# Kernel optimization log

Measured on AMD Instinct MI355X. Metric: run time of the kernel, lower is better.

Reference implementation:

```python
import jax, jax.numpy as jnp
import numpy as np
import math

B, S, D = 2, 512, 768
N_HEADS, HEAD = 12, 64
ALPHA = 32.0


def setup_inputs() -> dict:
    key = jax.random.key(0)
    ks = jax.random.split(key, 12)
    w_scale = 1.0 / math.sqrt(D)
    return {
        "hidden_states": jax.random.normal(ks[0], (B, S, D), jnp.float32),
        "attention_mask": jnp.zeros((B, 1, 1, S), jnp.float32),
        "rel_pos": jax.random.normal(ks[1], (B, S, S, HEAD), jnp.float32),
        "rel_2d_pos": jax.random.normal(ks[2], (B, S, S, HEAD), jnp.float32),
        "rel_2d_angle": jax.random.normal(ks[3], (B, S, S, HEAD), jnp.float32),
        "Wq": jax.random.normal(ks[4], (D, D), jnp.float32) * w_scale,
        "bq": jnp.zeros((D,), jnp.float32),
        "Wk": jax.random.normal(ks[5], (D, D), jnp.float32) * w_scale,
        "bk": jnp.zeros((D,), jnp.float32),
        "Wv": jax.random.normal(ks[6], (D, D), jnp.float32) * w_scale,
        "bv": jnp.zeros((D,), jnp.float32),
    }


def _heads(x):
    # (B,S,D) -> (B,N,S,HEAD)
    b, s, _ = x.shape
    return x.reshape(b, s, N_HEADS, HEAD).transpose(0, 2, 1, 3)


def reference(hidden_states, attention_mask, rel_pos, rel_2d_pos, rel_2d_angle,
              Wq, bq, Wk, bk, Wv, bv):
    q = _heads(hidden_states @ Wq.T + bq)
    k = _heads(hidden_states @ Wk.T + bk)
    v = _heads(hidden_states @ Wv.T + bv)

    qs = q / math.sqrt(HEAD)  # scaled query, (B,N,S,HEAD)
    scores = jnp.einsum('bnsh,bnkh->bnsk', qs, k)
    scores = scores + jnp.einsum('bnsh,bskh->bnsk', qs, rel_pos)
    scores = scores + jnp.einsum('bnsh,bskh->bnsk', qs, rel_2d_pos)
    scores = scores + jnp.einsum('bnsh,bskh->bnsk', qs, rel_2d_angle)
    scores = scores + attention_mask

    # cogview (PB-Relax) softmax: subtract per-row max of scores/alpha, rescale
    scaled = scores / ALPHA
    m = jnp.max(scaled, axis=-1, keepdims=True)
    probs = jax.nn.softmax((scaled - m) * ALPHA, axis=-1)

    ctx = jnp.einsum('bnsk,bnkh->bsnh', probs, v)  # (B,S,N,HEAD)
    return ctx.reshape(ctx.shape[0], ctx.shape[1], N_HEADS * HEAD)
```

## Files before the change

kernel.cpp:

```cpp
#include <hip/hip_runtime.h>

typedef __attribute__((ext_vector_type(8))) short short8;
typedef __attribute__((ext_vector_type(4))) float f32x4;

#define B_ 2
#define S_ 512
#define D_ 768
#define NH 12
#define HD 64

__device__ inline short f2bf(float f) {
    union { float f; unsigned u; } v; v.f = f;
    unsigned r = v.u + 0x7fffu + ((v.u >> 16) & 1u);
    return (short)(r >> 16);
}

__device__ __forceinline__ f32x4 ntload4(const float* p) {
    return __builtin_nontemporal_load((const f32x4*)p);
}

__global__ __launch_bounds__(256) void qkv_gemm(
    const float* __restrict__ hidden,
    const float* __restrict__ Wq, const float* __restrict__ Wk, const float* __restrict__ Wv,
    const float* __restrict__ bq, const float* __restrict__ bk, const float* __restrict__ bv,
    short* __restrict__ qbf, short* __restrict__ kbf, float* __restrict__ vws)
{
    __shared__ short hs[64 * 72];
    __shared__ short wt[64 * 72];

    const int mt = blockIdx.x, nt = blockIdx.y, mat = blockIdx.z;
    const int m0 = mt * 64, n0 = nt * 64;
    const float* W    = (mat == 0) ? Wq : ((mat == 1) ? Wk : Wv);
    const float* bias = (mat == 0) ? bq : ((mat == 1) ? bk : bv);

    const int tid = threadIdx.x;
    const int w = tid >> 6, l = tid & 63;
    const int sr = tid >> 2, sc = (tid & 3) * 16;

    f32x4 acc[4];
    #pragma unroll
    for (int i = 0; i < 4; ++i) acc[i] = (f32x4){0.f, 0.f, 0.f, 0.f};

    const int arow = (w * 16 + (l & 15)) * 72 + (l >> 4) * 8;

    for (int kt = 0; kt < 12; ++kt) {
        const int d0 = kt * 64;
        if (kt) __syncthreads();
        {
            const float4* sa = (const float4*)(hidden + (size_t)(m0 + sr) * D_ + d0 + sc);
            float4 x0 = sa[0], x1 = sa[1], x2 = sa[2], x3 = sa[3];
            short8 p0 = {f2bf(x0.x), f2bf(x0.y), f2bf(x0.z), f2bf(x0.w),
                         f2bf(x1.x), f2bf(x1.y), f2bf(x1.z), f2bf(x1.w)};
            short8 p1 = {f2bf(x2.x), f2bf(x2.y), f2bf(x2.z), f2bf(x2.w),
                         f2bf(x3.x), f2bf(x3.y), f2bf(x3.z), f2bf(x3.w)};
            *(short8*)&hs[sr * 72 + sc]     = p0;
            *(short8*)&hs[sr * 72 + sc + 8] = p1;
            const float4* sb = (const float4*)(W + (size_t)(n0 + sr) * D_ + d0 + sc);
            float4 y0 = sb[0], y1 = sb[1], y2 = sb[2], y3 = sb[3];
            short8 q0 = {f2bf(y0.x), f2bf(y0.y), f2bf(y0.z), f2bf(y0.w),
                         f2bf(y1.x), f2bf(y1.y), f2bf(y1.z), f2bf(y1.w)};
            short8 q1 = {f2bf(y2.x), f2bf(y2.y), f2bf(y2.z), f2bf(y2.w),
                         f2bf(y3.x), f2bf(y3.y), f2bf(y3.z), f2bf(y3.w)};
            *(short8*)&wt[sr * 72 + sc]     = q0;
            *(short8*)&wt[sr * 72 + sc + 8] = q1;
        }
        __syncthreads();
        short8 a0 = *(const short8*)&hs[arow];
        short8 a1 = *(const short8*)&hs[arow + 32];
        #pragma unroll
        for (int ct = 0; ct < 4; ++ct) {
            const int brow = (ct * 16 + (l & 15)) * 72 + (l >> 4) * 8;
            short8 b0 = *(const short8*)&wt[brow];
            short8 b1 = *(const short8*)&wt[brow + 32];
            acc[ct] = __builtin_amdgcn_mfma_f32_16x16x32_bf16(a0, b0, acc[ct], 0, 0, 0);
            acc[ct] = __builtin_amdgcn_mfma_f32_16x16x32_bf16(a1, b1, acc[ct], 0, 0, 0);
        }
    }

    #pragma unroll
    for (int ct = 0; ct < 4; ++ct) {
        #pragma unroll
        for (int rr = 0; rr < 4; ++rr) {
            const int m_l = w * 16 + (l >> 4) * 4 + rr;
            const int n_l = ct * 16 + (l & 15);
            const int m = m0 + m_l;
            const int b = m >> 9, s = m & 511;
            float v = acc[ct][rr] + bias[n0 + n_l];
            const size_t dst = (((size_t)(b * NH + nt) * S_) + s) * HD + n_l;
            if (mat == 0)      qbf[dst] = f2bf(v * 0.125f);
            else if (mat == 1) kbf[dst] = f2bf(v);
            else               vws[dst] = v;
        }
    }
}

__global__ __launch_bounds__(256) void score_rel(
    const short* __restrict__ qbf,
    const float* __restrict__ rel1, const float* __restrict__ rel2, const float* __restrict__ rel3,
    float* __restrict__ relsc)
{
    const int kt = blockIdx.x;
    const int s  = blockIdx.y;
    const int b  = blockIdx.z;
    const int tid = threadIdx.x;
    const int w = tid >> 6, l = tid & 63;

    const int rowsel = l & 15;
    const int hc     = (l >> 4) * 8;

    const int kc = kt * 4 + w;
    const size_t rbase = ((size_t)(b * S_ + s)) * S_ * HD;
    const size_t ro = rbase + (size_t)(kc * 16 + rowsel) * HD + hc;

    f32x4 p0a = ntload4(rel1 + ro);
    f32x4 p0b = ntload4(rel1 + ro + 4);
    f32x4 q0a = ntload4(rel1 + ro + 32);
    f32x4 q0b = ntload4(rel1 + ro + 36);
    f32x4 p1a = ntload4(rel2 + ro);
    f32x4 p1b = ntload4(rel2 + ro + 4);
    f32x4 q1a = ntload4(rel2 + ro + 32);
    f32x4 q1b = ntload4(rel2 + ro + 36);
    f32x4 p2a = ntload4(rel3 + ro);
    f32x4 p2b = ntload4(rel3 + ro + 4);
    f32x4 q2a = ntload4(rel3 + ro + 32);
    f32x4 q2b = ntload4(rel3 + ro + 36);

    short8 a0 = {0, 0, 0, 0, 0, 0, 0, 0};
    short8 a1 = {0, 0, 0, 0, 0, 0, 0, 0};
    if (rowsel < NH) {
        const short* qp = qbf + (((size_t)(b * NH + rowsel) * S_) + s) * HD;
        a0 = *(const short8*)(qp + hc);
        a1 = *(const short8*)(qp + hc + 32);
    }

    short8 b0 = {
        f2bf(p0a.x + p1a.x + p2a.x), f2bf(p0a.y + p1a.y + p2a.y),
        f2bf(p0a.z + p1a.z + p2a.z), f2bf(p0a.w + p1a.w + p2a.w),
        f2bf(p0b.x + p1b.x + p2b.x), f2bf(p0b.y + p1b.y + p2b.y),
        f2bf(p0b.z + p1b.z + p2b.z), f2bf(p0b.w + p1b.w + p2b.w)};
    short8 b1 = {
        f2bf(q0a.x + q1a.x + q2a.x), f2bf(q0a.y + q1a.y + q2a.y),
        f2bf(q0a.z + q1a.z + q2a.z), f2bf(q0a.w + q1a.w + q2a.w),
        f2bf(q0b.x + q1b.x + q2b.x), f2bf(q0b.y + q1b.y + q2b.y),
        f2bf(q0b.z + q1b.z + q2b.z), f2bf(q0b.w + q1b.w + q2b.w)};

    f32x4 acc = (f32x4){0.f, 0.f, 0.f, 0.f};
    acc = __builtin_amdgcn_mfma_f32_16x16x32_bf16(a0, b0, acc, 0, 0, 0);
    acc = __builtin_amdgcn_mfma_f32_16x16x32_bf16(a1, b1, acc, 0, 0, 0);

    const int kg = kc * 16 + rowsel;
    #pragma unroll
    for (int rr = 0; rr < 4; ++rr) {
        const int n = (l >> 4) * 4 + rr;
        if (n < NH) {
            float* p = relsc + (((size_t)(b * S_ + s)) * NH + n) * S_ + kg;
            __builtin_nontemporal_store(acc[rr], p);
        }
    }
}

__global__ __launch_bounds__(256) void smqkpv(
    const short* __restrict__ qbf, const short* __restrict__ kbf,
    const float* __restrict__ relsc, const float* __restrict__ mask,
    const float* __restrict__ vws, float* __restrict__ out)
{
    __shared__ float sc[16][520];

    const int st  = blockIdx.x;
    const int n   = blockIdx.y;
    const int b   = blockIdx.z;
    const int s0  = st * 16;
    const int tid = threadIdx.x;
    const int w = tid >> 6, l = tid & 63;

    const int arow = l & 15;
    const int g    = l >> 4;

    const short* qp = qbf + (((size_t)(b * NH + n) * S_) + s0 + arow) * HD + g * 8;
    short8 a0 = *(const short8*)(qp);
    short8 a1 = *(const short8*)(qp + 32);

    f32x4 acc[8];
    #pragma unroll
    for (int t = 0; t < 8; ++t) acc[t] = (f32x4){0.f, 0.f, 0.f, 0.f};

    #pragma unroll
    for (int t = 0; t < 8; ++t) {
        const int k0 = (w * 8 + t) * 16;
        const short* kp = kbf + (((size_t)(b * NH + n) * S_) + k0 + arow) * HD + g * 8;
        short8 b0 = *(const short8*)(kp);
        short8 b1 = *(const short8*)(kp + 32);
        acc[t] = __builtin_amdgcn_mfma_f32_16x16x32_bf16(a0, b0, acc[t], 0, 0, 0);
        acc[t] = __builtin_amdgcn_mfma_f32_16x16x32_bf16(a1, b1, acc[t], 0, 0, 0);
    }

    #pragma unroll
    for (int t = 0; t < 8; ++t) {
        const int k0 = (w * 8 + t) * 16;
        #pragma unroll
        for (int rr = 0; rr < 4; ++rr)
            sc[g * 4 + rr][k0 + arow] = acc[t][rr];
    }
    __syncthreads();

    #pragma unroll
    for (int j = 0; j < 8; ++j) {
        const int fidx = j * 256 + tid;
        const int row  = fidx >> 7;
        const int c4   = (fidx & 127) * 4;
        float4 r = *(const float4*)(relsc +
                    (((size_t)(b * S_ + s0 + row)) * NH + n) * S_ + c4);
        float4 mk = *(const float4*)(mask + b * S_ + c4);
        float4 cur = *(const float4*)&sc[row][c4];
        cur.x += r.x + mk.x; cur.y += r.y + mk.y;
        cur.z += r.z + mk.z; cur.w += r.w + mk.w;
        *(float4*)&sc[row][c4] = cur;
    }
    __syncthreads();

    const int lane = l;
    for (int r = 0; r < 4; ++r) {
        const int row = w * 4 + r;
        float vals[8];
        float m = -1e30f;
        #pragma unroll
        for (int i = 0; i < 8; ++i) { vals[i] = sc[row][lane + 64 * i]; m = fmaxf(m, vals[i]); }
        #pragma unroll
        for (int off = 32; off >= 1; off >>= 1) m = fmaxf(m, __shfl_xor(m, off));
        float sum = 0.f;
        #pragma unroll
        for (int i = 0; i < 8; ++i) { vals[i] = __expf(vals[i] - m); sum += vals[i]; }
        #pragma unroll
        for (int off = 32; off >= 1; off >>= 1) sum += __shfl_xor(sum, off);
        const float inv = 1.0f / sum;
        #pragma unroll
        for (int i = 0; i < 8; ++i) sc[row][lane + 64 * i] = vals[i] * inv;
    }
    __syncthreads();

    float pacc[4] = {0.f, 0.f, 0.f, 0.f};
    const float* vb = vws + (((size_t)(b * NH + n) * S_)) * HD + lane;
    for (int k = 0; k < S_; k += 4) {
        const float v0 = vb[(size_t)(k + 0) * HD];
        const float v1 = vb[(size_t)(k + 1) * HD];
        const float v2 = vb[(size_t)(k + 2) * HD];
        const float v3 = vb[(size_t)(k + 3) * HD];
        #pragma unroll
        for (int r = 0; r < 4; ++r) {
            float4 p = *(const float4*)&sc[w * 4 + r][k];
            pacc[r] += p.x * v0 + p.y * v1 + p.z * v2 + p.w * v3;
        }
    }
    #pragma unroll
    for (int r = 0; r < 4; ++r)
        out[((size_t)(b * S_ + s0 + w * 4 + r)) * D_ + n * HD + lane] = pacc[r];
}

extern "C" void kernel_launch(void* const* d_in, const int* in_sizes, int n_in,
                              void* d_out, int out_size, void* d_ws, size_t ws_size,
                              hipStream_t stream) {
    const float* hidden = (const float*)d_in[0];
    const float* mask   = (const float*)d_in[1];
    const float* rel1   = (const float*)d_in[2];
    const float* rel2   = (const float*)d_in[3];
    const float* rel3   = (const float*)d_in[4];
    const float* Wq     = (const float*)d_in[5];
    const float* bq     = (const float*)d_in[6];
    const float* Wk     = (const float*)d_in[7];
    const float* bk     = (const float*)d_in[8];
    const float* Wv     = (const float*)d_in[9];
    const float* bv     = (const float*)d_in[10];
    float* out = (float*)d_out;

    const size_t per = (size_t)B_ * NH * S_ * HD;
    short* qbf   = (short*)d_ws;
    short* kbf   = qbf + per;
    float* vws   = (float*)(kbf + per);
    float* relsc = vws + per;

    qkv_gemm<<<dim3(16, 12, 3), 256, 0, stream>>>(hidden, Wq, Wk, Wv, bq, bk, bv, qbf, kbf, vws);
    score_rel<<<dim3(8, S_, B_), 256, 0, stream>>>(qbf, rel1, rel2, rel3, relsc);
    smqkpv<<<dim3(S_ / 16, NH, B_), 256, 0, stream>>>(qbf, kbf, relsc, mask, vws, out);
}
```

Before: 143.5 us.

## Store V as transposed bf16 and compute PV with MFMA

V is now written in bf16 and transposed (head-dim major) through shared memory in the QKV GEMM epilogue. The attention kernel converts probabilities to bf16 in a separate LDS buffer and runs the PV product on 16x16x32 bf16 MFMA instead of a scalar FMA loop. The relative-score store also drops its nontemporal hint. This cuts V bandwidth and scalar ALU work in the softmax kernel, at the cost of extra LDS use and lower precision for probabilities and V.

```diff
diff --git a/kernel.cpp b/kernel.cpp
--- a/kernel.cpp
+++ b/kernel.cpp
@@ -23,7 +23,7 @@
     const float* __restrict__ hidden,
     const float* __restrict__ Wq, const float* __restrict__ Wk, const float* __restrict__ Wv,
     const float* __restrict__ bq, const float* __restrict__ bk, const float* __restrict__ bv,
-    short* __restrict__ qbf, short* __restrict__ kbf, float* __restrict__ vws)
+    short* __restrict__ qbf, short* __restrict__ kbf, short* __restrict__ vbf)
 {
     __shared__ short hs[64 * 72];
     __shared__ short wt[64 * 72];
@@ -77,19 +77,42 @@
         }
     }
 
-    #pragma unroll
-    for (int ct = 0; ct < 4; ++ct) {
-        #pragma unroll
-        for (int rr = 0; rr < 4; ++rr) {
-            const int m_l = w * 16 + (l >> 4) * 4 + rr;
-            const int n_l = ct * 16 + (l & 15);
-            const int m = m0 + m_l;
-            const int b = m >> 9, s = m & 511;
-            float v = acc[ct][rr] + bias[n0 + n_l];
-            const size_t dst = (((size_t)(b * NH + nt) * S_) + s) * HD + n_l;
-            if (mat == 0)      qbf[dst] = f2bf(v * 0.125f);
-            else if (mat == 1) kbf[dst] = f2bf(v);
-            else               vws[dst] = v;
+    if (mat == 2) {
+        __syncthreads();
+        #pragma unroll
+        for (int ct = 0; ct < 4; ++ct) {
+            #pragma unroll
+            for (int rr = 0; rr < 4; ++rr) {
+                const int m_l = w * 16 + (l >> 4) * 4 + rr;
+                const int n_l = ct * 16 + (l & 15);
+                hs[n_l * 68 + m_l] = f2bf(acc[ct][rr] + bias[n0 + n_l]);
+            }
+        }
+        __syncthreads();
+        const int b   = m0 >> 9;
+        const int s0b = m0 & 511;
+        #pragma unroll
+        for (int j = 0; j < 2; ++j) {
+            const int idx  = j * 256 + tid;
+            const int h    = idx >> 3;
+            const int sseg = (idx & 7) * 8;
+            short8 vv = *(const short8*)&hs[h * 68 + sseg];
+            *(short8*)(vbf + ((size_t)(b * NH + nt) * HD + h) * S_ + s0b + sseg) = vv;
+        }
+    } else {
+        #pragma unroll
+        for (int ct = 0; ct < 4; ++ct) {
+            #pragma unroll
+            for (int rr = 0; rr < 4; ++rr) {
+                const int m_l = w * 16 + (l >> 4) * 4 + rr;
+                const int n_l = ct * 16 + (l & 15);
+                const int m = m0 + m_l;
+                const int b = m >> 9, s = m & 511;
+                float v = acc[ct][rr] + bias[n0 + n_l];
+                const size_t dst = (((size_t)(b * NH + nt) * S_) + s) * HD + n_l;
+                if (mat == 0) qbf[dst] = f2bf(v * 0.125f);
+                else          kbf[dst] = f2bf(v);
+            }
         }
     }
 }
@@ -152,19 +175,18 @@
     #pragma unroll
     for (int rr = 0; rr < 4; ++rr) {
         const int n = (l >> 4) * 4 + rr;
-        if (n < NH) {
-            float* p = relsc + (((size_t)(b * S_ + s)) * NH + n) * S_ + kg;
-            __builtin_nontemporal_store(acc[rr], p);
-        }
+        if (n < NH)
+            relsc[(((size_t)(b * S_ + s)) * NH + n) * S_ + kg] = acc[rr];
     }
 }
 
 __global__ __launch_bounds__(256) void smqkpv(
     const short* __restrict__ qbf, const short* __restrict__ kbf,
     const float* __restrict__ relsc, const float* __restrict__ mask,
-    const float* __restrict__ vws, float* __restrict__ out)
+    const short* __restrict__ vbf, float* __restrict__ out)
 {
     __shared__ float sc[16][520];
+    __shared__ short pbf[16][520];
 
     const int st  = blockIdx.x;
     const int n   = blockIdx.y;
@@ -234,26 +256,23 @@
         for (int off = 32; off >= 1; off >>= 1) sum += __shfl_xor(sum, off);
         const float inv = 1.0f / sum;
         #pragma unroll
-        for (int i = 0; i < 8; ++i) sc[row][lane + 64 * i] = vals[i] * inv;
+        for (int i = 0; i < 8; ++i) pbf[row][lane + 64 * i] = f2bf(vals[i] * inv);
     }
     __syncthreads();
 
-    float pacc[4] = {0.f, 0.f, 0.f, 0.f};
-    const float* vb = vws + (((size_t)(b * NH + n) * S_)) * HD + lane;
-    for (int k = 0; k < S_; k += 4) {
-        const float v0 = vb[(size_t)(k + 0) * HD];
-        const float v1 = vb[(size_t)(k + 1) * HD];
-        const float v2 = vb[(size_t)(k + 2) * HD];
-        const float v3 = vb[(size_t)(k + 3) * HD];
-        #pragma unroll
-        for (int r = 0; r < 4; ++r) {
-            float4 p = *(const float4*)&sc[w * 4 + r][k];
-            pacc[r] += p.x * v0 + p.y * v1 + p.z * v2 + p.w * v3;
-        }
-    }
-    #pragma unroll
-    for (int r = 0; r < 4; ++r)
-        out[((size_t)(b * S_ + s0 + w * 4 + r)) * D_ + n * HD + lane] = pacc[r];
+    f32x4 pacc = (f32x4){0.f, 0.f, 0.f, 0.f};
+    const short* vrow = vbf + ((size_t)(b * NH + n) * HD + w * 16 + arow) * S_ + g * 8;
+    #pragma unroll
+    for (int kk = 0; kk < 16; ++kk) {
+        short8 aP = *(const short8*)&pbf[arow][kk * 32 + g * 8];
+        short8 bV = *(const short8*)(vrow + kk * 32);
+        pacc = __builtin_amdgcn_mfma_f32_16x16x32_bf16(aP, bV, pacc, 0, 0, 0);
+    }
+    #pragma unroll
+    for (int rr = 0; rr < 4; ++rr) {
+        const int srow = g * 4 + rr;
+        out[((size_t)(b * S_ + s0 + srow)) * D_ + n * HD + w * 16 + arow] = pacc[rr];
+    }
 }
 
 extern "C" void kernel_launch(void* const* d_in, const int* in_sizes, int n_in,
@@ -275,10 +294,10 @@
     const size_t per = (size_t)B_ * NH * S_ * HD;
     short* qbf   = (short*)d_ws;
     short* kbf   = qbf + per;
-    float* vws   = (float*)(kbf + per);
-    float* relsc = vws + per;
-
-    qkv_gemm<<<dim3(16, 12, 3), 256, 0, stream>>>(hidden, Wq, Wk, Wv, bq, bk, bv, qbf, kbf, vws);
+    short* vbf   = kbf + per;
+    float* relsc = (float*)(vbf + per);
+
+    qkv_gemm<<<dim3(16, 12, 3), 256, 0, stream>>>(hidden, Wq, Wk, Wv, bq, bk, bv, qbf, kbf, vbf);
     score_rel<<<dim3(8, S_, B_), 256, 0, stream>>>(qbf, rel1, rel2, rel3, relsc);
-    smqkpv<<<dim3(S_ / 16, NH, B_), 256, 0, stream>>>(qbf, kbf, relsc, mask, vws, out);
-}
+    smqkpv<<<dim3(S_ / 16, NH, B_), 256, 0, stream>>>(qbf, kbf, relsc, mask, vbf, out);
+}
```

Result: faster. 128.9 us (-10.2%).
